# Performance work log

Measured on AMD Instinct MI355X. Metric: run time of the kernel, lower is better.

The kernel has to match this reference:

```python
import jax, jax.numpy as jnp
import numpy as np


def setup_inputs() -> dict:
    key = jax.random.key(0)
    ks = jax.random.split(key, 8)
    B, De, Do, T, H, W = 4, 128, 512, 4, 30, 52
    s = 0.05  # weight init scale
    return {
        "m_in": jax.random.normal(ks[0], (B, De, T, H, W), jnp.float32),
        "m_out": jax.random.normal(ks[1], (B, Do, T, H, W), jnp.float32),
        "q_in": jax.random.normal(ks[2], (B, De, H, W), jnp.float32),
        "q_out": jax.random.normal(ks[3], (B, Do, H, W), jnp.float32),
        "wr": jax.random.normal(ks[4], (Do, 2 * Do), jnp.float32) * s,
        "br": jnp.zeros((Do,), jnp.float32),
        "wu": jax.random.normal(ks[5], (Do, 2 * Do), jnp.float32) * s,
        "bu": jnp.zeros((Do,), jnp.float32),
        "wc": jax.random.normal(ks[6], (Do, 2 * Do), jnp.float32) * s,
        "bc": jnp.zeros((Do,), jnp.float32),
    }


def reference(m_in, m_out, q_in, q_out, wr, br, wu, bu, wc, bc):
    B, De, T, H, W = m_in.shape
    Do = m_out.shape[1]
    PROP_LAYERS = 5

    # --- memory read: pairwise frame attention (bmm + softmax + bmm) ---
    # keys: all T memory frames flattened; queries: current frame.
    mi = m_in.reshape(B, De, T * H * W)            # [B, De, THW]
    qi = q_in.reshape(B, De, H * W)                # [B, De, HW]
    p = jnp.einsum('bdk,bdq->bkq', mi, qi) / (De ** 0.5)  # [B, THW, HW]
    p = jax.nn.softmax(p, axis=1)                  # softmax over memory locations (dim=1 in torch)
    mem = jnp.einsum('bok,bkq->boq', m_out.reshape(B, Do, T * H * W), p)
    mem = mem.reshape(B, Do, H, W)                 # mem_mean; identical every propagate layer

    # --- ConvGRU_h (kernel_size=1 => per-pixel linear gates) ---
    def conv1x1(w, b, x):
        return jnp.einsum('oc,bchw->bohw', w, x) + b[None, :, None, None]

    def gru(x, h):
        xh = jnp.concatenate([x, h], axis=1)                       # [B, 2*Do, H, W]
        r = jax.nn.sigmoid(conv1x1(wr, br, xh))
        u = jax.nn.sigmoid(conv1x1(wu, bu, xh))
        c = jnp.tanh(conv1x1(wc, bc, jnp.concatenate([x, r * h], axis=1)))
        return h * (1.0 - u) + u * c

    q0 = q_out
    q = q_out
    for _ in range(PROP_LAYERS):
        q = gru(q, mem)  # original: q_out = ConvGRU_h(q_out, mem_mean)
    return jnp.concatenate([q, q0], axis=1)  # [B, 2*Do, H, W]
```

## Files before the change

### kernel.cpp

```cpp
#include <hip/hip_runtime.h>
#include <hip/hip_bf16.h>
#include <math.h>

typedef unsigned short u16;
typedef __attribute__((ext_vector_type(8))) short bf16x8;
typedef __attribute__((ext_vector_type(4))) float f32x4;

__device__ __forceinline__ u16 f2bf(float f) {
  union { float f; unsigned u; } x; x.f = f;
  unsigned r = x.u + 0x7fffu + ((x.u >> 16) & 1u);
  return (u16)(r >> 16);
}
__device__ __forceinline__ float bf2f(u16 h) {
  union { unsigned u; float f; } x; x.u = ((unsigned)h) << 16;
  return x.f;
}
__device__ __forceinline__ float sigmf(float x) {
  x = fminf(fmaxf(x, -30.f), 30.f);
  return 1.f / (1.f + __expf(-x));
}
__device__ __forceinline__ float tanh_fast(float x) {
  x = fminf(fmaxf(x, -15.f), 15.f);
  float t = __expf(2.f * x);
  return (t - 1.f) / (t + 1.f);
}

template<int N> __device__ __forceinline__ void wait_vmcnt() {
  if constexpr (N == 0)      asm volatile("s_waitcnt vmcnt(0)" ::: "memory");
  else if constexpr (N == 4) asm volatile("s_waitcnt vmcnt(4)" ::: "memory");
  else if constexpr (N == 6) asm volatile("s_waitcnt vmcnt(6)" ::: "memory");
  else static_assert(N == 0 || N == 4 || N == 6, "add vmcnt case");
}

#define NB 4
#define DE 128
#define DO_ 512
#define HW 1560
#define THW 6240
#define NP 1664
#define KP 6272
#define PROP 5
#define PVSPLIT 7
#define PVKC 896

template<int MODE, int BMT, int BKT>
__device__ __forceinline__
void gemm_core(const u16* __restrict__ A, const u16* __restrict__ Bt,
               int K, int lda, int ldb, long a_bs, long b_bs,
               void* __restrict__ out0v, long o0_bs, int ld0,
               u16* __restrict__ out1, long o1_bs, int ld1,
               u16* __restrict__ out2, long o2_bs,
               const void* __restrict__ e0v, long e0_bs,
               const void* __restrict__ e1v, long e1_bs,
               const void* __restrict__ e2v, long e2_bs,
               const void* __restrict__ e3v, long e3_bs,
               int nvalid, float scale)
{
  constexpr int WR = BMT / 64;
  constexpr int WC = 4 / WR;
  constexpr int NF = 8 / WC;
  constexpr int KK = BKT / 32;
  constexpr int ASLOT = BMT * BKT / 8;
  constexpr int BSLOT = 128 * BKT / 8;
  constexpr int NISS = (ASLOT + BSLOT) / 256;
  constexpr int RSH = (BMT == 128) ? 7 : 6;
  __shared__ u16 lds[2][ASLOT + BSLOT][8];

  const int tid = threadIdx.x;
  const int wave = tid >> 6, lane = tid & 63;
  const int kg = lane >> 4, lr = lane & 15;
  const int wrw = wave / WC, wcw = wave % WC;
  const long b = blockIdx.z;
  const int m0 = blockIdx.x * BMT, n0 = blockIdx.y * 128;
  A += b * a_bs; Bt += b * b_bs;

  float* out0f = (float*)out0v;
  u16* out0h = (u16*)out0v;
  const float* e0f = (const float*)e0v;
  const u16* e0h = (const u16*)e0v;
  const u16* e1h = (const u16*)e1v;
  const u16* e2h = (const u16*)e2v;
  const u16* e3h = (const u16*)e3v;

  auto stage = [&](int buf, int kt) {
#pragma unroll
    for (int i = 0; i < NISS; ++i) {
      int s = tid + 256 * i;
      const u16* src;
      if (s < ASLOT) {
        int row = s & (BMT - 1), g = s >> RSH;
        src = A + (long)(m0 + row) * lda + kt + g * 8;
      } else {
        int s2 = s - ASLOT;
        int row = s2 & 127, g = s2 >> 7;
        src = Bt + (long)(n0 + row) * ldb + kt + g * 8;
      }
      __builtin_amdgcn_global_load_lds(
          (const __attribute__((address_space(1))) void*)src,
          (__attribute__((address_space(3))) void*)&lds[buf][wave * 64 + 256 * i][0],
          16, 0, 0);
    }
  };

  f32x4 acc[4][NF];
#pragma unroll
  for (int m = 0; m < 4; ++m)
#pragma unroll
    for (int n = 0; n < NF; ++n) acc[m][n] = (f32x4){0.f, 0.f, 0.f, 0.f};

  const int nt = K / BKT;
  stage(0, 0);
  for (int t = 0; t < nt; ++t) {
    int cur = t & 1;
    if (t + 1 < nt) {
      stage(cur ^ 1, (t + 1) * BKT);
      wait_vmcnt<NISS>();
    } else {
      wait_vmcnt<0>();
    }
    __builtin_amdgcn_s_barrier();
    bf16x8 af[KK][4], bfr[KK][NF];
#pragma unroll
    for (int kk = 0; kk < KK; ++kk) {
#pragma unroll
      for (int m = 0; m < 4; ++m)
        af[kk][m] = *(const bf16x8*)&lds[cur][(kk * 4 + kg) * BMT + wrw * 64 + m * 16 + lr][0];
#pragma unroll
      for (int n = 0; n < NF; ++n)
        bfr[kk][n] = *(const bf16x8*)&lds[cur][ASLOT + (kk * 4 + kg) * 128 + (wcw * NF + n) * 16 + lr][0];
    }
#pragma unroll
    for (int kk = 0; kk < KK; ++kk)
#pragma unroll
      for (int m = 0; m < 4; ++m)
#pragma unroll
        for (int n = 0; n < NF; ++n)
          acc[m][n] = __builtin_amdgcn_mfma_f32_16x16x32_bf16(af[kk][m], bfr[kk][n], acc[m][n], 0, 0, 0);
    __builtin_amdgcn_s_barrier();
  }

  if constexpr (MODE == 0) {
    float rs[4][4];
#pragma unroll
    for (int m = 0; m < 4; ++m)
#pragma unroll
      for (int j = 0; j < 4; ++j) rs[m][j] = 0.f;
#pragma unroll
    for (int m = 0; m < 4; ++m) {
      int rloc = wrw * 64 + m * 16 + kg * 4;
#pragma unroll
      for (int n = 0; n < NF; ++n) {
        int col = n0 + (wcw * NF + n) * 16 + lr;
#pragma unroll
        for (int j = 0; j < 4; ++j) {
          long row = m0 + rloc + j;
          float p = __expf(acc[m][n][j] * scale);
          bool valid = (col < nvalid);
          out1[b * o1_bs + row * ld1 + col] = valid ? f2bf(p) : (u16)0;
          rs[m][j] += valid ? p : 0.f;
        }
      }
    }
#pragma unroll
    for (int m = 0; m < 4; ++m)
#pragma unroll
      for (int j = 0; j < 4; ++j) {
#pragma unroll
        for (int msk = 1; msk < 16; msk <<= 1)
          rs[m][j] += __shfl_xor(rs[m][j], msk, 64);
      }
    float* zbuf = (float*)lds;
    if (lr == 0) {
#pragma unroll
      for (int m = 0; m < 4; ++m)
#pragma unroll
        for (int j = 0; j < 4; ++j)
          zbuf[wcw * 128 + wrw * 64 + m * 16 + kg * 4 + j] = rs[m][j];
    }
    __syncthreads();
    if (tid < 128)
      out0f[b * o0_bs + (long)blockIdx.y * NP + (m0 + tid)] = zbuf[tid] + zbuf[128 + tid];
    return;
  }

#pragma unroll
  for (int m = 0; m < 4; ++m) {
    int rloc = wrw * 64 + m * 16 + kg * 4;
#pragma unroll
    for (int n = 0; n < NF; ++n) {
      int col = n0 + (wcw * NF + n) * 16 + lr;
#pragma unroll
      for (int j = 0; j < 4; ++j) {
        long row = m0 + rloc + j;
        float v = acc[m][n][j];
        if constexpr (MODE == 2) {
          out1[b * o1_bs + row * ld1 + col] = f2bf(v + e0f[col]);
        } else if constexpr (MODE == 3) {
          if (col < 1024) {
            float gt = sigmf(v + bf2f(e0h[b * e0_bs + row * 1024 + col]));
            if (col < 512)
              out1[b * o1_bs + row * ld1 + 512 + col] =
                  f2bf(gt * bf2f(e1h[b * e1_bs + row * 512 + col]));
            else
              out0h[b * o0_bs + row * ld0 + (col - 512)] = f2bf(gt);
          } else {
            out2[b * o2_bs + row * 512 + (col - 1024)] = f2bf(v);
          }
        } else if constexpr (MODE == 4) {
          float cg = tanh_fast(v + bf2f(e3h[b * e3_bs + row * 512 + col]) + e0f[col]);
          float u = bf2f(e1h[b * e1_bs + row * 512 + col]);
          float mm = bf2f(e2h[b * e2_bs + row * 512 + col]);
          float x = mm * (1.f - u) + u * cg;
          out1[b * o1_bs + row * ld1 + col] = f2bf(x);
          if (out0f) out0f[b * o0_bs + row * ld0 + col] = x;
        }
      }
    }
  }
}

#define GEMM_ARGS                                                              \
  const u16* __restrict__ A, const u16* __restrict__ Bt, int K, int lda,       \
  int ldb, long a_bs, long b_bs, void* __restrict__ out0v, long o0_bs,         \
  int ld0, u16* __restrict__ out1, long o1_bs, int ld1,                        \
  u16* __restrict__ out2, long o2_bs,                                          \
  const void* __restrict__ e0v, long e0_bs, const void* __restrict__ e1v,      \
  long e1_bs, const void* __restrict__ e2v, long e2_bs,                        \
  const void* __restrict__ e3v, long e3_bs, int nvalid, float scale
#define GEMM_PASS A, Bt, K, lda, ldb, a_bs, b_bs, out0v, o0_bs, ld0, out1,     \
  o1_bs, ld1, out2, o2_bs, e0v, e0_bs, e1v, e1_bs, e2v, e2_bs, e3v, e3_bs,     \
  nvalid, scale

__global__ __launch_bounds__(256) void gk_scores(GEMM_ARGS) { gemm_core<0, 128, 32>(GEMM_PASS); }
__global__ __launch_bounds__(256) void gk_chru(GEMM_ARGS)   { gemm_core<2, 64, 64>(GEMM_PASS); }
__global__ __launch_bounds__(256) void gk_gates(GEMM_ARGS)  { gemm_core<3, 64, 64>(GEMM_PASS); }
__global__ __launch_bounds__(256) void gk_cand(GEMM_ARGS)   { gemm_core<4, 64, 64>(GEMM_PASS); }

__global__ __launch_bounds__(256, 2)
void gemm_pv(const u16* __restrict__ Pt, const u16* __restrict__ moutb,
             u16* __restrict__ Ppart)
{
  const int bid = blockIdx.x;
  const int xcd = bid & 7, i = bid >> 3;
  const int s = xcd * 91 + i;
  const int pair = s / 26, mb = s - pair * 26;
  const int b = pair / PVSPLIT, z = pair - b * PVSPLIT;
  const int m0 = mb * 64;
  const int k0 = z * PVKC;

  const u16* A = Pt + (long)b * NP * KP;
  const u16* B0;
  {
    const u16* Bb = moutb + (long)b * DO_ * KP;
    B0 = Bb + (long)((threadIdx.x >> 6) * 128 + (threadIdx.x & 15)) * KP +
         ((threadIdx.x & 63) >> 4) * 8;
  }

  __shared__ u16 lds[2][2048];
  const int tid = threadIdx.x;
  const int wave = tid >> 6, lane = tid & 63;
  const int kg = lane >> 4, lr = lane & 15;

  auto stage = [&](int buf, int kt) {
    int row = tid & 63, g = tid >> 6;
    const u16* src = A + (long)(m0 + row) * KP + kt + g * 8;
    __builtin_amdgcn_global_load_lds(
        (const __attribute__((address_space(1))) void*)src,
        (__attribute__((address_space(3))) void*)&lds[buf][(wave * 64) * 8],
        16, 0, 0);
  };

  f32x4 acc[4][8];
#pragma unroll
  for (int m = 0; m < 4; ++m)
#pragma unroll
    for (int n = 0; n < 8; ++n) acc[m][n] = (f32x4){0.f, 0.f, 0.f, 0.f};

  bf16x8 bra[8], brb[8];
#pragma unroll
  for (int n = 0; n < 8; ++n)
    bra[n] = *(const bf16x8*)&B0[(long)n * 16 * KP + k0];
  stage(0, k0);
  __syncthreads();

#define PV_STEP(BU, BL, T, CUR)                                                  \
  {                                                                              \
    if ((T) + 1 < 28) {                                                          \
      int ktn = k0 + ((T) + 1) * 32;                                             \
      _Pragma("unroll") for (int n = 0; n < 8; ++n)                              \
          BL[n] = *(const bf16x8*)&B0[(long)n * 16 * KP + ktn];                  \
      stage((CUR) ^ 1, ktn);                                                     \
    }                                                                            \
    bf16x8 af[4];                                                                \
    _Pragma("unroll") for (int m = 0; m < 4; ++m)                                \
        af[m] = *(const bf16x8*)&lds[CUR][(kg * 64 + m * 16 + lr) * 8];          \
    _Pragma("unroll") for (int m = 0; m < 4; ++m)                                \
        _Pragma("unroll") for (int n = 0; n < 8; ++n)                            \
            acc[m][n] = __builtin_amdgcn_mfma_f32_16x16x32_bf16(af[m], BU[n],    \
                                                                acc[m][n], 0, 0, 0); \
    __syncthreads();                                                             \
  }

  for (int tp = 0; tp < 14; ++tp) {
    PV_STEP(bra, brb, 2 * tp, 0);
    PV_STEP(brb, bra, 2 * tp + 1, 1);
  }
#undef PV_STEP

  u16* out = Ppart + (long)(b * PVSPLIT + z) * NP * DO_;
#pragma unroll
  for (int m = 0; m < 4; ++m) {
#pragma unroll
    for (int n = 0; n < 8; ++n) {
      int col = wave * 128 + n * 16 + lr;
#pragma unroll
      for (int j = 0; j < 4; ++j) {
        int row = m0 + m * 16 + kg * 4 + j;
        out[(long)row * DO_ + col] = f2bf(acc[m][n][j]);
      }
    }
  }
}

__global__ void k_transpose_cast(const float* __restrict__ in, u16* __restrict__ out,
                                 int R, int C, int Cp, int out_ld,
                                 long in_bs, long out_bs) {
  __shared__ float t[32][33];
  long b = blockIdx.z;
  int c0 = blockIdx.x * 32, r0 = blockIdx.y * 32;
  int tx = threadIdx.x, ty = threadIdx.y;
#pragma unroll
  for (int i = 0; i < 32; i += 8) {
    int r = r0 + ty + i, c = c0 + tx;
    t[ty + i][tx] = (r < R && c < C) ? in[b * in_bs + (long)r * C + c] : 0.f;
  }
  __syncthreads();
#pragma unroll
  for (int i = 0; i < 32; i += 8) {
    int c = c0 + ty + i, r = r0 + tx;
    if (c < Cp && r < R)
      out[b * out_bs + (long)c * out_ld + r] = f2bf(t[tx][ty + i]);
  }
}

__global__ void k_cast_pad(const float* __restrict__ in, u16* __restrict__ out,
                           int Cin, int Cout, long in_bs, long out_bs) {
  int c = blockIdx.x * 256 + threadIdx.x;
  int r = blockIdx.y;
  long b = blockIdx.z;
  if (c >= Cout) return;
  out[b * out_bs + (long)r * Cout + c] =
      (c < Cin) ? f2bf(in[b * in_bs + (long)r * Cin + c]) : (u16)0;
}

__global__ void k_build_w(const float* __restrict__ wr_, const float* __restrict__ wu_,
                          const float* __restrict__ wc_,
                          u16* __restrict__ wruh, u16* __restrict__ wruxc,
                          u16* __restrict__ wch) {
  int k = blockIdx.x * 256 + threadIdx.x;
  int m = blockIdx.y;
  if (k >= 512) return;
  if (m < 1024) {
    const float* src = (m < 512) ? wr_ : wu_;
    wruh[m * 512 + k] = f2bf(src[(m & 511) * 1024 + 512 + k]);
  } else if (m < 2560) {
    int n = m - 1024;
    const float* src = (n < 512) ? wr_ : ((n < 1024) ? wu_ : wc_);
    wruxc[n * 512 + k] = f2bf(src[(n & 511) * 1024 + k]);
  } else {
    int n = m - 2560;
    wch[n * 512 + k] = f2bf(wc_[n * 1024 + 512 + k]);
  }
}

__global__ void k_bias_ru(const float* __restrict__ br_, const float* __restrict__ bu_,
                          float* __restrict__ bias) {
  int i = blockIdx.x * 256 + threadIdx.x;
  if (i < 1024) bias[i] = (i < 512) ? br_[i] : bu_[i - 512];
}

__global__ void k_invz(const float* __restrict__ Zp, float* __restrict__ invZ) {
  int t = blockIdx.x * 256 + threadIdx.x;
  if (t >= NB * NP) return;
  int b = t / NP, q = t - b * NP;
  const float* base = Zp + (long)b * 49 * NP + q;
  float s = 0.f;
#pragma unroll
  for (int nb = 0; nb < 49; ++nb) s += base[(long)nb * NP];
  invZ[t] = 1.f / s;
}

__global__ void k_reduce_mem(const u16* __restrict__ Ppart, const float* __restrict__ invZ,
                             u16* __restrict__ memTb) {
  long t = (long)blockIdx.x * 256 + threadIdx.x;
  const long bs = (long)NP * DO_;
  if (t >= (long)NB * bs / 8) return;
  long flat = t * 8;
  int b = (int)(flat / bs);
  long r = flat - (long)b * bs;
  int q = (int)(r / DO_);
  float s[8];
#pragma unroll
  for (int e = 0; e < 8; ++e) s[e] = 0.f;
#pragma unroll
  for (int z = 0; z < PVSPLIT; ++z) {
    uint4 v = *(const uint4*)&Ppart[(long)(b * PVSPLIT + z) * bs + r];
    s[0] += bf2f((u16)(v.x & 0xffff)); s[1] += bf2f((u16)(v.x >> 16));
    s[2] += bf2f((u16)(v.y & 0xffff)); s[3] += bf2f((u16)(v.y >> 16));
    s[4] += bf2f((u16)(v.z & 0xffff)); s[5] += bf2f((u16)(v.z >> 16));
    s[6] += bf2f((u16)(v.w & 0xffff)); s[7] += bf2f((u16)(v.w >> 16));
  }
  float iz = invZ[b * NP + q];
  uint4 o;
  o.x = (unsigned)f2bf(s[0] * iz) | ((unsigned)f2bf(s[1] * iz) << 16);
  o.y = (unsigned)f2bf(s[2] * iz) | ((unsigned)f2bf(s[3] * iz) << 16);
  o.z = (unsigned)f2bf(s[4] * iz) | ((unsigned)f2bf(s[5] * iz) << 16);
  o.w = (unsigned)f2bf(s[6] * iz) | ((unsigned)f2bf(s[7] * iz) << 16);
  *(uint4*)&memTb[(long)b * bs + r] = o;
}

__global__ void k_out_q(const float* __restrict__ Qfin, float* __restrict__ dout) {
  __shared__ float t[32][33];
  long b = blockIdx.z;
  int q0 = blockIdx.x * 32, ch0 = blockIdx.y * 32;
  int tx = threadIdx.x, ty = threadIdx.y;
#pragma unroll
  for (int i = 0; i < 32; i += 8)
    t[ty + i][tx] = Qfin[b * ((long)NP * 512) + (long)(q0 + ty + i) * 512 + ch0 + tx];
  __syncthreads();
#pragma unroll
  for (int i = 0; i < 32; i += 8) {
    int ch = ch0 + ty + i, q = q0 + tx;
    if (q < HW)
      dout[b * ((long)1024 * HW) + (long)ch * HW + q] = t[tx][ty + i];
  }
}

__global__ void k_copy_q0(const float4* __restrict__ src, float4* __restrict__ dst) {
  int idx = blockIdx.x * 256 + threadIdx.x;
  long b = blockIdx.z;
  const long n4 = (long)DO_ * HW / 4;
  if (idx < n4)
    dst[b * ((long)1024 * HW / 4) + n4 + idx] = src[b * n4 + idx];
}

extern "C" void kernel_launch(void* const* d_in, const int* in_sizes, int n_in,
                              void* d_out, int out_size, void* d_ws, size_t ws_size,
                              hipStream_t stream) {
  const float* m_in  = (const float*)d_in[0];
  const float* m_out = (const float*)d_in[1];
  const float* q_in  = (const float*)d_in[2];
  const float* q_out = (const float*)d_in[3];
  const float* wr    = (const float*)d_in[4];
  const float* br    = (const float*)d_in[5];
  const float* wu    = (const float*)d_in[6];
  const float* bu    = (const float*)d_in[7];
  const float* wc    = (const float*)d_in[8];
  const float* bc    = (const float*)d_in[9];
  float* dout = (float*)d_out;

  char* p = (char*)d_ws;
  size_t off = 0;
  auto alloc = [&](size_t bytes) { void* r = p + off; off += (bytes + 255) & ~(size_t)255; return r; };
  u16*   miT    = (u16*)alloc((size_t)NB * KP * DE * 2);
  u16*   qiT    = (u16*)alloc((size_t)NB * NP * DE * 2);
  u16*   Pt     = (u16*)alloc((size_t)NB * NP * KP * 2);
  float* invZ   = (float*)alloc((size_t)NB * NP * 4);
  u16*   moutb  = (u16*)alloc((size_t)NB * DO_ * KP * 2);
  u16*   memTb  = (u16*)alloc((size_t)NB * NP * DO_ * 2);
  u16*   chru   = (u16*)alloc((size_t)NB * NP * 1024 * 2);
  u16*   U      = (u16*)alloc((size_t)NB * NP * DO_ * 2);
  u16*   XRb    = (u16*)alloc((size_t)NB * NP * 1024 * 2);
  float* Qfin   = (float*)alloc((size_t)NB * NP * DO_ * 4);
  u16*   XRa    = (u16*)alloc((size_t)NB * NP * 1024 * 2);
  u16*   Cx     = (u16*)alloc((size_t)NB * NP * 512 * 2);
  u16*   wruh   = (u16*)alloc((size_t)1024 * 512 * 2);
  u16*   wruxc  = (u16*)alloc((size_t)1536 * 512 * 2);
  u16*   wch    = (u16*)alloc((size_t)512 * 512 * 2);
  float* biasru = (float*)alloc((size_t)1024 * 4);
  u16*   Ppart  = (u16*)chru;
  float* Zp     = (float*)memTb;
  if (off > ws_size) return;

  k_build_w<<<dim3(2, 3072), 256, 0, stream>>>(wr, wu, wc, wruh, wruxc, wch);
  k_bias_ru<<<dim3(4), 256, 0, stream>>>(br, bu, biasru);
  k_cast_pad<<<dim3(25, 512, NB), 256, 0, stream>>>(
      m_out, moutb, THW, KP, (long)DO_ * THW, (long)DO_ * KP);
  k_transpose_cast<<<dim3(196, 4, NB), dim3(32, 8), 0, stream>>>(
      m_in, miT, DE, THW, KP, DE, (long)DE * THW, (long)KP * DE);
  k_transpose_cast<<<dim3(52, 4, NB), dim3(32, 8), 0, stream>>>(
      q_in, qiT, DE, HW, NP, DE, (long)DE * HW, (long)NP * DE);
  k_transpose_cast<<<dim3(52, 16, NB), dim3(32, 8), 0, stream>>>(
      q_out, XRa, DO_, HW, NP, 1024, (long)DO_ * HW, (long)NP * 1024);

  gk_scores<<<dim3(13, 49, NB), 256, 0, stream>>>(
      qiT, miT, DE, DE, DE, (long)NP * DE, (long)KP * DE,
      Zp, (long)49 * NP, 0, Pt, (long)NP * KP, KP, nullptr, 0,
      nullptr, 0, nullptr, 0, nullptr, 0, nullptr, 0, THW, 0.08838834764831845f);
  k_invz<<<dim3(26), 256, 0, stream>>>(Zp, invZ);

  gemm_pv<<<dim3(728), 256, 0, stream>>>(Pt, moutb, Ppart);
  k_reduce_mem<<<dim3(1664), 256, 0, stream>>>(Ppart, invZ, memTb);

  gk_chru<<<dim3(26, 8, NB), 256, 0, stream>>>(
      memTb, wruh, DO_, DO_, DO_, (long)NP * DO_, 0,
      nullptr, 0, 0, chru, (long)NP * 1024, 1024, nullptr, 0,
      biasru, 0, nullptr, 0, nullptr, 0, nullptr, 0, 0, 0.f);

  u16* xr[2] = {XRa, XRb};
  for (int l = 0; l < PROP; ++l) {
    u16* cur = xr[l & 1];
    u16* nxt = xr[(l + 1) & 1];
    gk_gates<<<dim3(26, 12, NB), 256, 0, stream>>>(
        cur, wruxc, DO_, 1024, DO_, (long)NP * 1024, 0,
        U, (long)NP * DO_, DO_, cur, (long)NP * 1024, 1024,
        Cx, (long)NP * 512,
        chru, (long)NP * 1024, memTb, (long)NP * DO_, nullptr, 0,
        nullptr, 0, 0, 0.f);
    gk_cand<<<dim3(26, 4, NB), 256, 0, stream>>>(
        cur + 512, wch, DO_, 1024, DO_, (long)NP * 1024, 0,
        (l == PROP - 1) ? (void*)Qfin : nullptr, (long)NP * DO_, DO_,
        nxt, (long)NP * 1024, 1024, nullptr, 0,
        bc, 0, U, (long)NP * DO_, memTb, (long)NP * DO_,
        Cx, (long)NP * 512, 0, 0.f);
  }

  k_out_q<<<dim3(49, 16, NB), dim3(32, 8), 0, stream>>>(Qfin, dout);
  k_copy_q0<<<dim3(780, 1, NB), 256, 0, stream>>>((const float4*)q_out, (float4*)dout);
}
```

Before: 656.7 us.

## Stage PV B operand through LDS with async loads; vectorize m_out cast

The PV GEMM now loads the m_out (B) tile straight into LDS with global_load_lds, alongside the A tile, into double-buffered shared arrays. Explicit vmcnt waits and raw s_barrier calls replace __syncthreads, and the old register-prefetched B fragments are removed. The m_out cast-and-pad kernel now handles four elements per thread using float4 loads and packed bf16 stores. The aim is better overlap and coalescing of global loads, at the cost of much more LDS per block, which could lower occupancy, and more reliance on manual wait counts.

```diff
diff --git a/kernel.cpp b/kernel.cpp
--- a/kernel.cpp
+++ b/kernel.cpp
@@ -29,7 +29,8 @@
   if constexpr (N == 0)      asm volatile("s_waitcnt vmcnt(0)" ::: "memory");
   else if constexpr (N == 4) asm volatile("s_waitcnt vmcnt(4)" ::: "memory");
   else if constexpr (N == 6) asm volatile("s_waitcnt vmcnt(6)" ::: "memory");
-  else static_assert(N == 0 || N == 4 || N == 6, "add vmcnt case");
+  else if constexpr (N == 9) asm volatile("s_waitcnt vmcnt(9)" ::: "memory");
+  else static_assert(N == 0 || N == 4 || N == 6 || N == 9, "add vmcnt case");
 }
 
 #define NB 4
@@ -249,25 +250,32 @@
   const int k0 = z * PVKC;
 
   const u16* A = Pt + (long)b * NP * KP;
-  const u16* B0;
-  {
-    const u16* Bb = moutb + (long)b * DO_ * KP;
-    B0 = Bb + (long)((threadIdx.x >> 6) * 128 + (threadIdx.x & 15)) * KP +
-         ((threadIdx.x & 63) >> 4) * 8;
-  }
-
-  __shared__ u16 lds[2][2048];
+  const u16* Bb = moutb + (long)b * DO_ * KP;
+
+  __shared__ u16 ldsA[2][256][8];
+  __shared__ u16 ldsB[2][2048][8];
+
   const int tid = threadIdx.x;
   const int wave = tid >> 6, lane = tid & 63;
   const int kg = lane >> 4, lr = lane & 15;
 
+  const u16* asrc = A + (long)(m0 + (tid & 63)) * KP + k0 + (tid >> 6) * 8;
+
   auto stage = [&](int buf, int kt) {
-    int row = tid & 63, g = tid >> 6;
-    const u16* src = A + (long)(m0 + row) * KP + kt + g * 8;
     __builtin_amdgcn_global_load_lds(
-        (const __attribute__((address_space(1))) void*)src,
-        (__attribute__((address_space(3))) void*)&lds[buf][(wave * 64) * 8],
+        (const __attribute__((address_space(1))) void*)(asrc + kt),
+        (__attribute__((address_space(3))) void*)&ldsA[buf][wave * 64][0],
         16, 0, 0);
+#pragma unroll
+    for (int i2 = 0; i2 < 8; ++i2) {
+      int s2 = tid + 256 * i2;
+      int row = s2 & 511, g = s2 >> 9;
+      const u16* src = Bb + (long)row * KP + k0 + kt + g * 8;
+      __builtin_amdgcn_global_load_lds(
+          (const __attribute__((address_space(1))) void*)src,
+          (__attribute__((address_space(3))) void*)&ldsB[buf][wave * 64 + 256 * i2][0],
+          16, 0, 0);
+    }
   };
 
   f32x4 acc[4][8];
@@ -276,36 +284,30 @@
 #pragma unroll
     for (int n = 0; n < 8; ++n) acc[m][n] = (f32x4){0.f, 0.f, 0.f, 0.f};
 
-  bf16x8 bra[8], brb[8];
-#pragma unroll
-  for (int n = 0; n < 8; ++n)
-    bra[n] = *(const bf16x8*)&B0[(long)n * 16 * KP + k0];
-  stage(0, k0);
-  __syncthreads();
-
-#define PV_STEP(BU, BL, T, CUR)                                                  \
-  {                                                                              \
-    if ((T) + 1 < 28) {                                                          \
-      int ktn = k0 + ((T) + 1) * 32;                                             \
-      _Pragma("unroll") for (int n = 0; n < 8; ++n)                              \
-          BL[n] = *(const bf16x8*)&B0[(long)n * 16 * KP + ktn];                  \
-      stage((CUR) ^ 1, ktn);                                                     \
-    }                                                                            \
-    bf16x8 af[4];                                                                \
-    _Pragma("unroll") for (int m = 0; m < 4; ++m)                                \
-        af[m] = *(const bf16x8*)&lds[CUR][(kg * 64 + m * 16 + lr) * 8];          \
-    _Pragma("unroll") for (int m = 0; m < 4; ++m)                                \
-        _Pragma("unroll") for (int n = 0; n < 8; ++n)                            \
-            acc[m][n] = __builtin_amdgcn_mfma_f32_16x16x32_bf16(af[m], BU[n],    \
-                                                                acc[m][n], 0, 0, 0); \
-    __syncthreads();                                                             \
-  }
-
-  for (int tp = 0; tp < 14; ++tp) {
-    PV_STEP(bra, brb, 2 * tp, 0);
-    PV_STEP(brb, bra, 2 * tp + 1, 1);
-  }
-#undef PV_STEP
+  stage(0, 0);
+  for (int t = 0; t < 28; ++t) {
+    int cur = t & 1;
+    if (t + 1 < 28) {
+      stage(cur ^ 1, (t + 1) * 32);
+      wait_vmcnt<9>();
+    } else {
+      wait_vmcnt<0>();
+    }
+    __builtin_amdgcn_s_barrier();
+    bf16x8 af[4], bf[8];
+#pragma unroll
+    for (int m = 0; m < 4; ++m)
+      af[m] = *(const bf16x8*)&ldsA[cur][kg * 64 + m * 16 + lr][0];
+#pragma unroll
+    for (int n = 0; n < 8; ++n)
+      bf[n] = *(const bf16x8*)&ldsB[cur][kg * 512 + wave * 128 + n * 16 + lr][0];
+#pragma unroll
+    for (int m = 0; m < 4; ++m)
+#pragma unroll
+      for (int n = 0; n < 8; ++n)
+        acc[m][n] = __builtin_amdgcn_mfma_f32_16x16x32_bf16(af[m], bf[n], acc[m][n], 0, 0, 0);
+    __builtin_amdgcn_s_barrier();
+  }
 
   u16* out = Ppart + (long)(b * PVSPLIT + z) * NP * DO_;
 #pragma unroll
@@ -343,14 +345,19 @@
   }
 }
 
-__global__ void k_cast_pad(const float* __restrict__ in, u16* __restrict__ out,
-                           int Cin, int Cout, long in_bs, long out_bs) {
-  int c = blockIdx.x * 256 + threadIdx.x;
+__global__ void k_cast_pad4(const float* __restrict__ in, u16* __restrict__ out,
+                            int Cin, int Cout, long in_bs, long out_bs) {
+  int c4 = (blockIdx.x * 256 + threadIdx.x) * 4;
   int r = blockIdx.y;
   long b = blockIdx.z;
-  if (c >= Cout) return;
-  out[b * out_bs + (long)r * Cout + c] =
-      (c < Cin) ? f2bf(in[b * in_bs + (long)r * Cin + c]) : (u16)0;
+  if (c4 >= Cout) return;
+  uint2 o = {0u, 0u};
+  if (c4 < Cin) {
+    float4 v = *(const float4*)&in[b * in_bs + (long)r * Cin + c4];
+    o.x = (unsigned)f2bf(v.x) | ((unsigned)f2bf(v.y) << 16);
+    o.y = (unsigned)f2bf(v.z) | ((unsigned)f2bf(v.w) << 16);
+  }
+  *(uint2*)&out[b * out_bs + (long)r * Cout + c4] = o;
 }
 
 __global__ void k_build_w(const float* __restrict__ wr_, const float* __restrict__ wu_,
@@ -484,7 +491,7 @@
 
   k_build_w<<<dim3(2, 3072), 256, 0, stream>>>(wr, wu, wc, wruh, wruxc, wch);
   k_bias_ru<<<dim3(4), 256, 0, stream>>>(br, bu, biasru);
-  k_cast_pad<<<dim3(25, 512, NB), 256, 0, stream>>>(
+  k_cast_pad4<<<dim3(7, 512, NB), 256, 0, stream>>>(
       m_out, moutb, THW, KP, (long)DO_ * THW, (long)DO_ * KP);
   k_transpose_cast<<<dim3(196, 4, NB), dim3(32, 8), 0, stream>>>(
       m_in, miT, DE, THW, KP, DE, (long)DE * THW, (long)KP * DE);
```

Measured after the change: 742.7 us. 1.13x slower.
